# Kernel tuning notes

Hardware: AMD Instinct MI355X
Metric: run time of the kernel (lower is better)

## Reference

```python
import jax, jax.numpy as jnp
import numpy as np

N, E = 50000, 800000
IN_DIM, OUT_DIM, EDGE_DIM = 128, 128, 6
LN_EPS = 1e-5


def setup_inputs() -> dict:
    key = jax.random.key(0)
    ks = jax.random.split(key, 9)
    w = lambda k, sh: (jax.random.normal(k, sh, jnp.float32) * 0.05)
    return {
        "x": jax.random.normal(ks[0], (N, IN_DIM), jnp.float32),
        "edge_attr": jax.random.normal(ks[1], (E, EDGE_DIM), jnp.float32),
        "Wn": w(ks[2], (IN_DIM, OUT_DIM)),
        "bn": jnp.zeros((OUT_DIM,), jnp.float32),
        "We": w(ks[3], (EDGE_DIM, OUT_DIM)),
        "be": jnp.zeros((OUT_DIM,), jnp.float32),
        "Wm": w(ks[4], (2 * OUT_DIM, OUT_DIM)),
        "bm": jnp.zeros((OUT_DIM,), jnp.float32),
        "gamma": jnp.ones((OUT_DIM,), jnp.float32),
        "beta": jnp.zeros((OUT_DIM,), jnp.float32),
        "edge_index": jax.random.randint(ks[5], (2, E), 0, N, jnp.int32),
    }


def reference(x, edge_attr, Wn, bn, We, be, Wm, bm, gamma, beta, edge_index):
    row, col = edge_index[0], edge_index[1]
    x_t = x @ Wn + bn                                  # [N, D]
    e_t = edge_attr @ We + be                          # [E, D]
    msgs = jnp.concatenate([x_t[col], e_t], axis=-1)   # gather + concat [E, 2D]
    msgs = jax.nn.relu(msgs @ Wm + bm)                 # [E, D]
    agg = jax.ops.segment_sum(msgs, row, num_segments=N)            # scatter_add
    deg = jax.ops.segment_sum(jnp.ones((E,), jnp.float32), row, num_segments=N)
    out = agg / jnp.clip(deg, 1.0)[:, None] + x_t      # mean-normalize + residual
    mu = out.mean(axis=-1, keepdims=True)
    var = out.var(axis=-1, keepdims=True)
    return (out - mu) * jax.lax.rsqrt(var + LN_EPS) * gamma + beta
```

## Files before the change

### kernel.cpp

```cpp
#include <hip/hip_runtime.h>
#include <hip/hip_bf16.h>

#define D 128
#define EDGE_DIM 6
#define LN_EPS 1e-5f
#define HIST_BLOCKS 2048

typedef __attribute__((ext_vector_type(8))) short short8;
typedef __attribute__((ext_vector_type(4))) float f32x4;
typedef __attribute__((ext_vector_type(2))) float f32x2;

static __device__ __forceinline__ float bf_lo(unsigned u) { return __uint_as_float(u << 16); }
static __device__ __forceinline__ float bf_hi(unsigned u) { return __uint_as_float(u & 0xffff0000u); }
static __device__ __forceinline__ unsigned short f2bf(float f) {
    __hip_bfloat16 h = __float2bfloat16(f);
    return *reinterpret_cast<unsigned short*>(&h);
}

__global__ __launch_bounds__(128)
void setup_all(const float* __restrict__ Wn, const float* __restrict__ bn,
               const float* __restrict__ We, const float* __restrict__ be,
               const float* __restrict__ Wm, const float* __restrict__ bm,
               const int* __restrict__ ei, int E,
               float* __restrict__ Wnm, float* __restrict__ bnm,
               float* __restrict__ Wc, float* __restrict__ bc,
               int* __restrict__ cnt) {
    const int b = blockIdx.x;
    const int d = threadIdx.x;
    if (b < 128) {
        float acc = 0.f;
#pragma unroll 8
        for (int j = 0; j < D; ++j)
            acc = fmaf(Wn[b * D + j], Wm[j * D + d], acc);
        Wnm[b * D + d] = acc;
    } else if (b == 128) {
        float acc = 0.f;
#pragma unroll 8
        for (int j = 0; j < D; ++j)
            acc = fmaf(bn[j], Wm[j * D + d], acc);
        bnm[d] = acc;
    } else if (b < 135) {
        const int k = b - 129;
        float acc = 0.f;
#pragma unroll 8
        for (int j = 0; j < D; ++j)
            acc = fmaf(We[k * D + j], Wm[(D + j) * D + d], acc);
        Wc[k * D + d] = acc;
    } else if (b == 135) {
        float acc = bm[d];
#pragma unroll 8
        for (int j = 0; j < D; ++j)
            acc = fmaf(be[j], Wm[(D + j) * D + d], acc);
        bc[d] = acc;
    } else {
        for (int i = (b - 136) * 128 + d; i < E; i += HIST_BLOCKS * 128)
            atomicAdd(&cnt[ei[i]], 1);
    }
}

__global__ __launch_bounds__(1024)
void scan_pack(const int* __restrict__ cnt, int* __restrict__ start,
               int* __restrict__ cur, int* __restrict__ cursor, int n, int nscan,
               const float* __restrict__ Wn, const float* __restrict__ Wnm,
               unsigned short* __restrict__ Wb) {
    const int tid = threadIdx.x;
    if ((int)blockIdx.x >= nscan) {
        const int idx = ((int)blockIdx.x - nscan) * 1024 + tid;
        if (idx < 4096) {
            const int lane = idx & 63;
            const int s = (idx >> 6) & 3;
            const int ct = (idx >> 8) & 7;
            const int mat = idx >> 11;
            const float* W = mat ? Wnm : Wn;
            const int col = ct * 16 + (lane & 15);
            const int k0 = (lane >> 4) * 8 + 32 * s;
            short8 v;
#pragma unroll
            for (int j = 0; j < 8; ++j)
                v[j] = (short)f2bf(W[(size_t)(k0 + j) * D + col]);
            *reinterpret_cast<short8*>(Wb + (size_t)idx * 8) = v;
        }
        return;
    }
    __shared__ int wsum[16];
    __shared__ int sbase;
    const int lane = tid & 63, wid = tid >> 6;
    const int i = blockIdx.x * 1024 + tid;
    const int v = (i < n) ? cnt[i] : 0;
    int x = v;
#pragma unroll
    for (int off = 1; off < 64; off <<= 1) {
        int t = __shfl_up(x, off);
        if (lane >= off) x += t;
    }
    if (lane == 63) wsum[wid] = x;
    __syncthreads();
    if (wid == 0) {
        int w = (lane < 16) ? wsum[lane] : 0;
#pragma unroll
        for (int off = 1; off < 16; off <<= 1) {
            int t = __shfl_up(w, off);
            if (lane >= off) w += t;
        }
        if (lane < 16) wsum[lane] = w;
    }
    __syncthreads();
    const int total = wsum[15];
    if (tid == 0) sbase = atomicAdd(cursor, total);
    __syncthreads();
    const int woff = (wid > 0) ? wsum[wid - 1] : 0;
    if (i < n) {
        const int sv = sbase + woff + x - v;
        start[i] = sv;
        cur[i] = sv;
    }
}

__global__ __launch_bounds__(256)
void scatter_rec(const int* __restrict__ ei, int E, const float* __restrict__ ea,
                 int* __restrict__ cur, uint4* __restrict__ rec) {
    __shared__ unsigned sR[2048 * 3];
    const int tid = threadIdx.x;
    const int base = blockIdx.x * 2048;
    const int nrec = min(2048, E - base);
    const float2* ea2 = reinterpret_cast<const float2*>(ea);
    for (int i = tid; i < nrec * 3; i += 256) {
        float2 p = ea2[(size_t)base * 3 + i];
        sR[i] = (unsigned)f2bf(p.x) | ((unsigned)f2bf(p.y) << 16);
    }
    __syncthreads();

    int rows[8], cols[8], pos[8];
#pragma unroll
    for (int it = 0; it < 8; ++it) {
        const int e = base + it * 256 + tid;
        const bool val = e < E;
        rows[it] = val ? ei[e] : -1;
        cols[it] = val ? ei[E + e] : 0;
    }
#pragma unroll
    for (int it = 0; it < 8; ++it)
        if (rows[it] >= 0) pos[it] = atomicAdd(&cur[rows[it]], 1);
#pragma unroll
    for (int it = 0; it < 8; ++it)
        if (rows[it] >= 0) {
            const int le = (it * 256 + tid) * 3;
            rec[pos[it]] = make_uint4((unsigned)cols[it], sR[le], sR[le + 1], sR[le + 2]);
        }
}

__global__ __launch_bounds__(64)
void gemm_mfma(const float* __restrict__ x, const unsigned short* __restrict__ Wb,
               const float* __restrict__ bn, const float* __restrict__ bnm,
               unsigned short* __restrict__ xtb, unsigned short* __restrict__ hb,
               int nrows) {
    const int lane = threadIdx.x;
    const int row16 = lane & 15;
    const int kgrp = lane >> 4;
    const int t = blockIdx.x;

    float biasA[8], biasB[8];
#pragma unroll
    for (int ct = 0; ct < 8; ++ct) {
        biasA[ct] = bn[ct * 16 + row16];
        biasB[ct] = bnm[ct * 16 + row16];
    }

    const int ra = t * 16 + row16;
    const bool rv = ra < nrows;
    short8 a[4];
#pragma unroll
    for (int s = 0; s < 4; ++s) {
        const float* xp = x + (size_t)ra * D + kgrp * 8 + 32 * s;
        float4 u0 = rv ? *reinterpret_cast<const float4*>(xp)
                       : make_float4(0.f, 0.f, 0.f, 0.f);
        float4 u1 = rv ? *reinterpret_cast<const float4*>(xp + 4)
                       : make_float4(0.f, 0.f, 0.f, 0.f);
        a[s][0] = (short)f2bf(u0.x); a[s][1] = (short)f2bf(u0.y);
        a[s][2] = (short)f2bf(u0.z); a[s][3] = (short)f2bf(u0.w);
        a[s][4] = (short)f2bf(u1.x); a[s][5] = (short)f2bf(u1.y);
        a[s][6] = (short)f2bf(u1.z); a[s][7] = (short)f2bf(u1.w);
    }
    const int rw0 = t * 16 + kgrp * 4;
#pragma unroll
    for (int mat = 0; mat < 2; ++mat) {
        unsigned short* out = mat ? hb : xtb;
#pragma unroll
        for (int ct = 0; ct < 8; ++ct) {
            f32x4 acc = {0.f, 0.f, 0.f, 0.f};
#pragma unroll
            for (int s = 0; s < 4; ++s) {
                short8 bfr = *reinterpret_cast<const short8*>(
                    Wb + (size_t)((((mat * 8 + ct) * 4 + s) * 64 + lane)) * 8);
                acc = __builtin_amdgcn_mfma_f32_16x16x32_bf16(a[s], bfr, acc, 0, 0, 0);
            }
            const float bsc = mat ? biasB[ct] : biasA[ct];
            const int dcol = ct * 16 + row16;
#pragma unroll
            for (int j = 0; j < 4; ++j) {
                const int r = rw0 + j;
                if (r < nrows) out[(size_t)r * D + dcol] = f2bf(acc[j] + bsc);
            }
        }
    }
}

__global__ __launch_bounds__(256)
void aggregate_ln(const unsigned* __restrict__ h,
                  const int* __restrict__ start, const int* __restrict__ cnt,
                  const uint4* __restrict__ rec,
                  const float* __restrict__ Wc, const float* __restrict__ bc,
                  const unsigned* __restrict__ xtb,
                  const float* __restrict__ gamma, const float* __restrict__ beta,
                  float* __restrict__ out, int nnode) {
    const int lane = threadIdx.x & 63;
    const int wid = threadIdx.x >> 6;

    f32x2 wc[EDGE_DIM];
#pragma unroll
    for (int k = 0; k < EDGE_DIM; ++k)
        wc[k] = reinterpret_cast<const f32x2*>(Wc)[k * 64 + lane];
    const f32x2 bc2 = reinterpret_cast<const f32x2*>(bc)[lane];
    const f32x2 g = reinterpret_cast<const f32x2*>(gamma)[lane];
    const f32x2 bb = reinterpret_cast<const f32x2*>(beta)[lane];

    for (int n = blockIdx.x * 4 + wid; n < nnode; n += gridDim.x * 4) {
        const int s = start[n];
        const int c = cnt[n];
        const unsigned xu = xtb[(unsigned)(n * 64 + lane)];
        f32x2 axy = {0.f, 0.f};
        for (int ibase = 0; ibase < c; ibase += 64) {
            const int m = min(64, c - ibase);
            uint4 rc = make_uint4(0, 0, 0, 0);
            if (lane < m) rc = rec[(size_t)(s + ibase) + lane];
            auto LDH = [&](int j) -> unsigned {
                const int jc = min(j, m - 1);
                const unsigned colj = (unsigned)__builtin_amdgcn_readlane((int)rc.x, jc);
                const unsigned* hrow = h + ((size_t)colj << 6);
                return hrow[lane];
            };
            auto COMP = [&](int j, unsigned hv) {
                const unsigned b01 = (unsigned)__builtin_amdgcn_readlane((int)rc.y, j);
                const unsigned b23 = (unsigned)__builtin_amdgcn_readlane((int)rc.z, j);
                const unsigned b45 = (unsigned)__builtin_amdgcn_readlane((int)rc.w, j);
                f32x2 e01, e23, e45, hx, mA, mB;
                e01[0] = bf_lo(b01); e01[1] = bf_hi(b01);
                e23[0] = bf_lo(b23); e23[1] = bf_hi(b23);
                e45[0] = bf_lo(b45); e45[1] = bf_hi(b45);
                hx[0] = bf_lo(hv); hx[1] = bf_hi(hv);
                asm("v_pk_add_f32 %0, %1, %2" : "=v"(mA) : "v"(bc2), "v"(hx));
                asm("v_pk_mul_f32 %0, %1, %2 op_sel:[1,0] op_sel_hi:[1,1]"
                    : "=v"(mB) : "s"(e01), "v"(wc[1]));
                asm("v_pk_fma_f32 %0, %1, %2, %0 op_sel:[0,0,0] op_sel_hi:[0,1,1]"
                    : "+v"(mA) : "s"(e01), "v"(wc[0]));
                asm("v_pk_fma_f32 %0, %1, %2, %0 op_sel:[1,0,0] op_sel_hi:[1,1,1]"
                    : "+v"(mB) : "s"(e23), "v"(wc[3]));
                asm("v_pk_fma_f32 %0, %1, %2, %0 op_sel:[0,0,0] op_sel_hi:[0,1,1]"
                    : "+v"(mA) : "s"(e23), "v"(wc[2]));
                asm("v_pk_fma_f32 %0, %1, %2, %0 op_sel:[1,0,0] op_sel_hi:[1,1,1]"
                    : "+v"(mB) : "s"(e45), "v"(wc[5]));
                asm("v_pk_fma_f32 %0, %1, %2, %0 op_sel:[0,0,0] op_sel_hi:[0,1,1]"
                    : "+v"(mA) : "s"(e45), "v"(wc[4]));
                asm("v_pk_add_f32 %0, %0, %1" : "+v"(mA) : "v"(mB));
                axy[0] += fmaxf(mA[0], 0.f);
                axy[1] += fmaxf(mA[1], 0.f);
            };
            unsigned h0 = LDH(0), h1 = LDH(1), h2 = LDH(2), h3 = LDH(3),
                     h4 = LDH(4), h5 = LDH(5), h6 = LDH(6), h7 = LDH(7);
            int i = 0;
            for (; i + 8 <= m; i += 8) {
                COMP(i + 0, h0); h0 = LDH(i + 8);
                COMP(i + 1, h1); h1 = LDH(i + 9);
                COMP(i + 2, h2); h2 = LDH(i + 10);
                COMP(i + 3, h3); h3 = LDH(i + 11);
                COMP(i + 4, h4); h4 = LDH(i + 12);
                COMP(i + 5, h5); h5 = LDH(i + 13);
                COMP(i + 6, h6); h6 = LDH(i + 14);
                COMP(i + 7, h7); h7 = LDH(i + 15);
            }
            if (i + 0 < m) COMP(i + 0, h0);
            if (i + 1 < m) COMP(i + 1, h1);
            if (i + 2 < m) COMP(i + 2, h2);
            if (i + 3 < m) COMP(i + 3, h3);
            if (i + 4 < m) COMP(i + 4, h4);
            if (i + 5 < m) COMP(i + 5, h5);
            if (i + 6 < m) COMP(i + 6, h6);
        }
        const float inv = 1.0f / fmaxf((float)c, 1.0f);
        float o0 = fmaf(axy[0], inv, bf_lo(xu));
        float o1 = fmaf(axy[1], inv, bf_hi(xu));
        float s1 = o0 + o1, s2 = o0 * o0 + o1 * o1;
#pragma unroll
        for (int off = 32; off; off >>= 1) {
            s1 += __shfl_xor(s1, off);
            s2 += __shfl_xor(s2, off);
        }
        const float mean = s1 * (1.0f / D);
        const float var = s2 * (1.0f / D) - mean * mean;
        const float rstd = rsqrtf(var + LN_EPS);
        float2 r;
        r.x = (o0 - mean) * rstd * g[0] + bb[0];
        r.y = (o1 - mean) * rstd * g[1] + bb[1];
        reinterpret_cast<float2*>(out)[(size_t)n * 64 + lane] = r;
    }
}

extern "C" void kernel_launch(void* const* d_in, const int* in_sizes, int n_in,
                              void* d_out, int out_size, void* d_ws, size_t ws_size,
                              hipStream_t stream) {
    const float* x     = (const float*)d_in[0];
    const float* eattr = (const float*)d_in[1];
    const float* Wn    = (const float*)d_in[2];
    const float* bn    = (const float*)d_in[3];
    const float* We    = (const float*)d_in[4];
    const float* be    = (const float*)d_in[5];
    const float* Wm    = (const float*)d_in[6];
    const float* bm    = (const float*)d_in[7];
    const float* gamma = (const float*)d_in[8];
    const float* beta  = (const float*)d_in[9];
    const int*   ei    = (const int*)d_in[10];

    const int N = in_sizes[0] / D;
    const int E = in_sizes[10] / 2;

    char* ws = (char*)d_ws;
    unsigned short* xtb = (unsigned short*)ws; ws += (size_t)N * D * 2;
    unsigned short* hb  = (unsigned short*)ws; ws += (size_t)N * D * 2;
    int* ints = (int*)ws;                      ws += (size_t)(N + 4) * 4;
    int* cnt = ints;
    int* cursor = ints + N;
    int* cur    = (int*)ws;                    ws += (size_t)N * 4;
    int* startv = (int*)ws;                    ws += (size_t)N * 4;
    uint4* rec  = (uint4*)ws;                  ws += (size_t)E * 16;
    float* Wnm  = (float*)ws;                  ws += (size_t)D * D * 4;
    float* bnm  = (float*)ws;                  ws += (size_t)D * 4;
    float* Wc   = (float*)ws;                  ws += (size_t)EDGE_DIM * D * 4;
    float* bcv  = (float*)ws;                  ws += (size_t)D * 4;
    unsigned short* Wb = (unsigned short*)ws;  ws += (size_t)4096 * 8 * 2;

    const int nscan = (N + 1023) / 1024;
    const int ntile = (N + 15) / 16;

    hipMemsetAsync(ints, 0, (size_t)(N + 4) * 4, stream);

    setup_all<<<136 + HIST_BLOCKS, 128, 0, stream>>>(Wn, bn, We, be, Wm, bm, ei, E,
                                                     Wnm, bnm, Wc, bcv, cnt);
    scan_pack<<<nscan + 4, 1024, 0, stream>>>(cnt, startv, cur, cursor, N, nscan,
                                              Wn, Wnm, Wb);
    scatter_rec<<<(E + 2047) / 2048, 256, 0, stream>>>(ei, E, eattr, cur, rec);
    gemm_mfma<<<ntile, 64, 0, stream>>>(x, Wb, bn, bnm, xtb, hb, N);
    aggregate_ln<<<(N + 3) / 4, 256, 0, stream>>>((const unsigned*)hb, startv, cnt, rec,
                                                  Wc, bcv, (const unsigned*)xtb,
                                                  gamma, beta, (float*)d_out, N);
}
```

Baseline: 173.2 us.

## Store gathered node features as fp8 and restructure aggregation to four edges per wave

The per-node message table h is now stored as fp8 instead of bf16, which halves the bytes fetched by the random per-edge gather. The aggregation kernel changes layout: each wave handles four edges at once, with each lane covering 8 feature columns of one edge. Edge records are distributed with ds_bpermute, and the edge-feature projection is computed with bf16 dot2 instructions. Partial sums are reduced across quarter-waves before the layernorm. The lower fp8 precision on gathered features risks failing the accuracy tolerance, and the wave now does more per-lane work and more cross-lane shuffles.

```diff
diff --git a/kernel.cpp b/kernel.cpp
--- a/kernel.cpp
+++ b/kernel.cpp
@@ -15,6 +15,21 @@
 static __device__ __forceinline__ unsigned short f2bf(float f) {
     __hip_bfloat16 h = __float2bfloat16(f);
     return *reinterpret_cast<unsigned short*>(&h);
+}
+static __device__ __forceinline__ float dot2bf(unsigned a, unsigned b, float c) {
+    float d;
+    asm("v_dot2_f32_bf16 %0, %1, %2, %3" : "=v"(d) : "v"(a), "v"(b), "v"(c));
+    return d;
+}
+static __device__ __forceinline__ f32x2 cvt2_fp8(unsigned w) {
+    f32x2 r;
+    asm("v_cvt_pk_f32_fp8 %0, %1" : "=v"(r) : "v"(w));
+    return r;
+}
+static __device__ __forceinline__ unsigned f2fp8(float f) {
+    unsigned u;
+    asm("v_cvt_pk_fp8_f32 %0, %1, %2" : "=v"(u) : "v"(f), "v"(0.0f));
+    return u & 0xffu;
 }
 
 __global__ __launch_bounds__(128)
@@ -152,7 +167,7 @@
 __global__ __launch_bounds__(64)
 void gemm_mfma(const float* __restrict__ x, const unsigned short* __restrict__ Wb,
                const float* __restrict__ bn, const float* __restrict__ bnm,
-               unsigned short* __restrict__ xtb, unsigned short* __restrict__ hb,
+               unsigned short* __restrict__ xtb, unsigned char* __restrict__ hb,
                int nrows) {
     const int lane = threadIdx.x;
     const int row16 = lane & 15;
@@ -184,7 +199,6 @@
     const int rw0 = t * 16 + kgrp * 4;
 #pragma unroll
     for (int mat = 0; mat < 2; ++mat) {
-        unsigned short* out = mat ? hb : xtb;
 #pragma unroll
         for (int ct = 0; ct < 8; ++ct) {
             f32x4 acc = {0.f, 0.f, 0.f, 0.f};
@@ -199,14 +213,19 @@
 #pragma unroll
             for (int j = 0; j < 4; ++j) {
                 const int r = rw0 + j;
-                if (r < nrows) out[(size_t)r * D + dcol] = f2bf(acc[j] + bsc);
+                if (r < nrows) {
+                    if (mat == 0)
+                        xtb[(size_t)r * D + dcol] = f2bf(acc[j] + bsc);
+                    else
+                        hb[(size_t)r * D + dcol] = (unsigned char)f2fp8(acc[j] + bsc);
+                }
             }
         }
     }
 }
 
 __global__ __launch_bounds__(256)
-void aggregate_ln(const unsigned* __restrict__ h,
+void aggregate_ln(const unsigned char* __restrict__ h8,
                   const int* __restrict__ start, const int* __restrict__ cnt,
                   const uint4* __restrict__ rec,
                   const float* __restrict__ Wc, const float* __restrict__ bc,
@@ -215,93 +234,111 @@
                   float* __restrict__ out, int nnode) {
     const int lane = threadIdx.x & 63;
     const int wid = threadIdx.x >> 6;
-
-    f32x2 wc[EDGE_DIM];
-#pragma unroll
-    for (int k = 0; k < EDGE_DIM; ++k)
-        wc[k] = reinterpret_cast<const f32x2*>(Wc)[k * 64 + lane];
-    const f32x2 bc2 = reinterpret_cast<const f32x2*>(bc)[lane];
-    const f32x2 g = reinterpret_cast<const f32x2*>(gamma)[lane];
-    const f32x2 bb = reinterpret_cast<const f32x2*>(beta)[lane];
+    const int d0 = (lane & 15) * 8;
+    const int qsel = lane >> 4;
+
+    unsigned wcp[3][8];
+    float bcf[8], gf[8], bf[8];
+#pragma unroll
+    for (int p = 0; p < 3; ++p)
+#pragma unroll
+        for (int d = 0; d < 8; ++d) {
+            unsigned lo = f2bf(Wc[(2 * p) * D + d0 + d]);
+            unsigned hi = f2bf(Wc[(2 * p + 1) * D + d0 + d]);
+            wcp[p][d] = lo | (hi << 16);
+        }
+#pragma unroll
+    for (int d = 0; d < 8; ++d) {
+        bcf[d] = bc[d0 + d];
+        gf[d] = gamma[d0 + d];
+        bf[d] = beta[d0 + d];
+    }
 
     for (int n = blockIdx.x * 4 + wid; n < nnode; n += gridDim.x * 4) {
         const int s = start[n];
         const int c = cnt[n];
-        const unsigned xu = xtb[(unsigned)(n * 64 + lane)];
-        f32x2 axy = {0.f, 0.f};
+        float a8[8] = {0.f, 0.f, 0.f, 0.f, 0.f, 0.f, 0.f, 0.f};
         for (int ibase = 0; ibase < c; ibase += 64) {
             const int m = min(64, c - ibase);
+            const int mq = (m + 3) >> 2;
             uint4 rc = make_uint4(0, 0, 0, 0);
             if (lane < m) rc = rec[(size_t)(s + ibase) + lane];
-            auto LDH = [&](int j) -> unsigned {
-                const int jc = min(j, m - 1);
-                const unsigned colj = (unsigned)__builtin_amdgcn_readlane((int)rc.x, jc);
-                const unsigned* hrow = h + ((size_t)colj << 6);
-                return hrow[lane];
+            auto SLOT = [&](int qj) -> int { return min(qj * 4 + qsel, m - 1) << 2; };
+            auto LDQ = [&](int qj) -> uint2 {
+                const unsigned col =
+                    (unsigned)__builtin_amdgcn_ds_bpermute(SLOT(qj), (int)rc.x);
+                return *reinterpret_cast<const uint2*>(
+                    h8 + (size_t)((col << 7) | (unsigned)d0));
             };
-            auto COMP = [&](int j, unsigned hv) {
-                const unsigned b01 = (unsigned)__builtin_amdgcn_readlane((int)rc.y, j);
-                const unsigned b23 = (unsigned)__builtin_amdgcn_readlane((int)rc.z, j);
-                const unsigned b45 = (unsigned)__builtin_amdgcn_readlane((int)rc.w, j);
-                f32x2 e01, e23, e45, hx, mA, mB;
-                e01[0] = bf_lo(b01); e01[1] = bf_hi(b01);
-                e23[0] = bf_lo(b23); e23[1] = bf_hi(b23);
-                e45[0] = bf_lo(b45); e45[1] = bf_hi(b45);
-                hx[0] = bf_lo(hv); hx[1] = bf_hi(hv);
-                asm("v_pk_add_f32 %0, %1, %2" : "=v"(mA) : "v"(bc2), "v"(hx));
-                asm("v_pk_mul_f32 %0, %1, %2 op_sel:[1,0] op_sel_hi:[1,1]"
-                    : "=v"(mB) : "s"(e01), "v"(wc[1]));
-                asm("v_pk_fma_f32 %0, %1, %2, %0 op_sel:[0,0,0] op_sel_hi:[0,1,1]"
-                    : "+v"(mA) : "s"(e01), "v"(wc[0]));
-                asm("v_pk_fma_f32 %0, %1, %2, %0 op_sel:[1,0,0] op_sel_hi:[1,1,1]"
-                    : "+v"(mB) : "s"(e23), "v"(wc[3]));
-                asm("v_pk_fma_f32 %0, %1, %2, %0 op_sel:[0,0,0] op_sel_hi:[0,1,1]"
-                    : "+v"(mA) : "s"(e23), "v"(wc[2]));
-                asm("v_pk_fma_f32 %0, %1, %2, %0 op_sel:[1,0,0] op_sel_hi:[1,1,1]"
-                    : "+v"(mB) : "s"(e45), "v"(wc[5]));
-                asm("v_pk_fma_f32 %0, %1, %2, %0 op_sel:[0,0,0] op_sel_hi:[0,1,1]"
-                    : "+v"(mA) : "s"(e45), "v"(wc[4]));
-                asm("v_pk_add_f32 %0, %0, %1" : "+v"(mA) : "v"(mB));
-                axy[0] += fmaxf(mA[0], 0.f);
-                axy[1] += fmaxf(mA[1], 0.f);
+            auto QCOMP = [&](int qj, uint2 hv) {
+                const int sl = SLOT(qj);
+                const unsigned b01 = (unsigned)__builtin_amdgcn_ds_bpermute(sl, (int)rc.y);
+                const unsigned b23 = (unsigned)__builtin_amdgcn_ds_bpermute(sl, (int)rc.z);
+                const unsigned b45 = (unsigned)__builtin_amdgcn_ds_bpermute(sl, (int)rc.w);
+                f32x2 h01 = cvt2_fp8(hv.x), h23 = cvt2_fp8(hv.x >> 16);
+                f32x2 h45 = cvt2_fp8(hv.y), h67 = cvt2_fp8(hv.y >> 16);
+                const float hd[8] = {h01[0], h01[1], h23[0], h23[1],
+                                     h45[0], h45[1], h67[0], h67[1]};
+                const float keep = (qj * 4 + qsel < m) ? 1.0f : 0.0f;
+#pragma unroll
+                for (int d = 0; d < 8; ++d) {
+                    float t = bcf[d] + hd[d];
+                    t = dot2bf(b01, wcp[0][d], t);
+                    t = dot2bf(b23, wcp[1][d], t);
+                    t = dot2bf(b45, wcp[2][d], t);
+                    a8[d] = fmaf(keep, fmaxf(t, 0.0f), a8[d]);
+                }
             };
-            unsigned h0 = LDH(0), h1 = LDH(1), h2 = LDH(2), h3 = LDH(3),
-                     h4 = LDH(4), h5 = LDH(5), h6 = LDH(6), h7 = LDH(7);
-            int i = 0;
-            for (; i + 8 <= m; i += 8) {
-                COMP(i + 0, h0); h0 = LDH(i + 8);
-                COMP(i + 1, h1); h1 = LDH(i + 9);
-                COMP(i + 2, h2); h2 = LDH(i + 10);
-                COMP(i + 3, h3); h3 = LDH(i + 11);
-                COMP(i + 4, h4); h4 = LDH(i + 12);
-                COMP(i + 5, h5); h5 = LDH(i + 13);
-                COMP(i + 6, h6); h6 = LDH(i + 14);
-                COMP(i + 7, h7); h7 = LDH(i + 15);
+            uint2 hq0 = {0, 0}, hq1 = {0, 0}, hq2 = {0, 0}, hq3 = {0, 0};
+            hq0 = LDQ(0);
+            if (1 < mq) hq1 = LDQ(1);
+            if (2 < mq) hq2 = LDQ(2);
+            if (3 < mq) hq3 = LDQ(3);
+            for (int q = 0; q < 16; q += 4) {
+                if (q >= mq) break;
+                { QCOMP(q + 0, hq0); if (q + 4 < mq) hq0 = LDQ(q + 4); }
+                if (q + 1 < mq) { QCOMP(q + 1, hq1); if (q + 5 < mq) hq1 = LDQ(q + 5); }
+                if (q + 2 < mq) { QCOMP(q + 2, hq2); if (q + 6 < mq) hq2 = LDQ(q + 6); }
+                if (q + 3 < mq) { QCOMP(q + 3, hq3); if (q + 7 < mq) hq3 = LDQ(q + 7); }
             }
-            if (i + 0 < m) COMP(i + 0, h0);
-            if (i + 1 < m) COMP(i + 1, h1);
-            if (i + 2 < m) COMP(i + 2, h2);
-            if (i + 3 < m) COMP(i + 3, h3);
-            if (i + 4 < m) COMP(i + 4, h4);
-            if (i + 5 < m) COMP(i + 5, h5);
-            if (i + 6 < m) COMP(i + 6, h6);
+        }
+#pragma unroll
+        for (int d = 0; d < 8; ++d) {
+            a8[d] += __shfl_xor(a8[d], 16);
+            a8[d] += __shfl_xor(a8[d], 32);
         }
         const float inv = 1.0f / fmaxf((float)c, 1.0f);
-        float o0 = fmaf(axy[0], inv, bf_lo(xu));
-        float o1 = fmaf(axy[1], inv, bf_hi(xu));
-        float s1 = o0 + o1, s2 = o0 * o0 + o1 * o1;
-#pragma unroll
-        for (int off = 32; off; off >>= 1) {
+        const uint4 xq = *reinterpret_cast<const uint4*>(xtb + ((size_t)n << 6) + (d0 >> 1));
+        float o[8];
+        o[0] = fmaf(a8[0], inv, bf_lo(xq.x)); o[1] = fmaf(a8[1], inv, bf_hi(xq.x));
+        o[2] = fmaf(a8[2], inv, bf_lo(xq.y)); o[3] = fmaf(a8[3], inv, bf_hi(xq.y));
+        o[4] = fmaf(a8[4], inv, bf_lo(xq.z)); o[5] = fmaf(a8[5], inv, bf_hi(xq.z));
+        o[6] = fmaf(a8[6], inv, bf_lo(xq.w)); o[7] = fmaf(a8[7], inv, bf_hi(xq.w));
+        float s1 = 0.f, s2 = 0.f;
+#pragma unroll
+        for (int d = 0; d < 8; ++d) { s1 += o[d]; s2 += o[d] * o[d]; }
+#pragma unroll
+        for (int off = 1; off <= 8; off <<= 1) {
             s1 += __shfl_xor(s1, off);
             s2 += __shfl_xor(s2, off);
         }
         const float mean = s1 * (1.0f / D);
         const float var = s2 * (1.0f / D) - mean * mean;
         const float rstd = rsqrtf(var + LN_EPS);
-        float2 r;
-        r.x = (o0 - mean) * rstd * g[0] + bb[0];
-        r.y = (o1 - mean) * rstd * g[1] + bb[1];
-        reinterpret_cast<float2*>(out)[(size_t)n * 64 + lane] = r;
+        if (lane < 16) {
+            float4 r0, r1;
+            r0.x = (o[0] - mean) * rstd * gf[0] + bf[0];
+            r0.y = (o[1] - mean) * rstd * gf[1] + bf[1];
+            r0.z = (o[2] - mean) * rstd * gf[2] + bf[2];
+            r0.w = (o[3] - mean) * rstd * gf[3] + bf[3];
+            r1.x = (o[4] - mean) * rstd * gf[4] + bf[4];
+            r1.y = (o[5] - mean) * rstd * gf[5] + bf[5];
+            r1.z = (o[6] - mean) * rstd * gf[6] + bf[6];
+            r1.w = (o[7] - mean) * rstd * gf[7] + bf[7];
+            float4* op = reinterpret_cast<float4*>(out + (size_t)n * D + d0);
+            op[0] = r0;
+            op[1] = r1;
+        }
     }
 }
 
@@ -325,7 +362,7 @@
 
     char* ws = (char*)d_ws;
     unsigned short* xtb = (unsigned short*)ws; ws += (size_t)N * D * 2;
-    unsigned short* hb  = (unsigned short*)ws; ws += (size_t)N * D * 2;
+    unsigned char*  hb  = (unsigned char*)ws;  ws += (size_t)N * D;
     int* ints = (int*)ws;                      ws += (size_t)(N + 4) * 4;
     int* cnt = ints;
     int* cursor = ints + N;
@@ -349,7 +386,7 @@
                                               Wn, Wnm, Wb);
     scatter_rec<<<(E + 2047) / 2048, 256, 0, stream>>>(ei, E, eattr, cur, rec);
     gemm_mfma<<<ntile, 64, 0, stream>>>(x, Wb, bn, bnm, xtb, hb, N);
-    aggregate_ln<<<(N + 3) / 4, 256, 0, stream>>>((const unsigned*)hb, startv, cnt, rec,
+    aggregate_ln<<<(N + 3) / 4, 256, 0, stream>>>(hb, startv, cnt, rec,
                                                   Wc, bcv, (const unsigned*)xtb,
                                                   gamma, beta, (float*)d_out, N);
 }
```

After: 183.5 us. 5.9% more time.
